# Kernel optimization log

Measured on AMD Instinct MI355X. Metric: run time of the kernel, lower is better.

## Reference

```python
import jax, jax.numpy as jnp
import numpy as np

PATCH = 16  # conv kernel size == stride


def _patch_embed(im, W, b):
    # im: (B, C, H, W) NCHW; W: (hidden, C, s, s); returns (B, h, w, hidden)
    out = jax.lax.conv_general_dilated(
        im, W, window_strides=(PATCH, PATCH), padding='VALID',
        dimension_numbers=('NCHW', 'OIHW', 'NCHW'))
    out = out + b[None, :, None, None]
    return jnp.transpose(out, (0, 2, 3, 1))  # (B, h, w, hidden)


def setup_inputs() -> dict:
    key = jax.random.key(0)
    k1, k2, k3, k4 = jax.random.split(key, 4)
    B, C, H, Wd = 64, 3, 224, 224
    hidden = 384
    x = jax.random.normal(k1, (B, C, H, Wd), dtype=jnp.float32)
    y = jax.random.normal(k2, (B, C, H, Wd), dtype=jnp.float32)
    fan_in = C * PATCH * PATCH
    bound = 1.0 / np.sqrt(fan_in)
    W = jax.random.uniform(k3, (hidden, C, PATCH, PATCH), dtype=jnp.float32,
                           minval=-bound, maxval=bound)
    b = jax.random.uniform(k4, (hidden,), dtype=jnp.float32,
                           minval=-bound, maxval=bound)
    return {'x': x, 'y': y, 'W': W, 'b': b}


def reference(x, y, W, b):
    B = x.shape[0]
    xp = _patch_embed(x, W, b)  # (B, h, w, C)
    yp = _patch_embed(y, W, b)  # (B, h, w, C)
    h, w = xp.shape[1], xp.shape[2]
    logp = jax.nn.log_softmax(xp, axis=-1)          # (B, h, w, C)
    q = jax.lax.stop_gradient(jax.nn.softmax(yp, axis=-1))  # detached targets
    # CE[i, j] = mean over (h, w) of -(q_j * logp_i).sum(-1)
    # Faithful factorization of the (B, B, h, w, C) broadcast in the original.
    CE = -jnp.einsum('ihwc,jhwc->ij', logp, q) / (h * w)  # (B, B)
    close = jnp.trace(CE) / B
    far = (CE.sum() - jnp.trace(CE)) / (B * B - B)
    return close / far
```

## Files before the change

### kernel.cpp

```cpp
#include <hip/hip_runtime.h>

#define HID   384
#define K_PE  768
#define IMGST 150528
#define POS   196

typedef unsigned short ushort_t;
using f32x4  = __attribute__((ext_vector_type(4))) float;
using short8 = __attribute__((ext_vector_type(8))) short;

__device__ __forceinline__ unsigned bfpack(float lo, float hi) {
    union { float f; unsigned u; } a, b; a.f = lo; b.f = hi;
    unsigned ra = (a.u + 0x7fffu + ((a.u >> 16) & 1u)) >> 16;
    unsigned rb = (b.u + 0x7fffu + ((b.u >> 16) & 1u)) & 0xffff0000u;
    return ra | rb;
}

__global__ __launch_bounds__(256) void prep(const float* __restrict__ W,
                                            ushort_t* __restrict__ Wfrag,
                                            float* __restrict__ scal) {
    const int t = blockIdx.x * 256 + threadIdx.x;
    if (t < 4) scal[t] = 0.f;
    const int n  = t / 96;
    const int ko = t - n * 96;
    const float4 a  = *(const float4*)(W + (size_t)n * K_PE + ko * 8);
    const float4 bb = *(const float4*)(W + (size_t)n * K_PE + ko * 8 + 4);
    uint4 pq;
    pq.x = bfpack(a.x, a.y);   pq.y = bfpack(a.z, a.w);
    pq.z = bfpack(bb.x, bb.y); pq.w = bfpack(bb.z, bb.w);
    const int nt    = n >> 4;
    const int kc    = ko >> 2;
    const int lanew = (ko & 3) * 16 + (n & 15);
    ((uint4*)Wfrag)[(nt * 24 + kc) * 64 + lanew] = pq;
}

__global__ __launch_bounds__(256, 2) void pef(
    const float* __restrict__ x, const float* __restrict__ y,
    const ushort_t* __restrict__ Wfrag, const float* __restrict__ bias,
    float* __restrict__ scal, float* __restrict__ Lg, float* __restrict__ Qg) {
    const int blk = blockIdx.x;
    const int pi  = blk >> 5;
    const int ig  = blk & 31;

    __shared__ __align__(16) ushort_t As[2][1792];
    __shared__ float Smx[4][32], Ssx[4][32], Smy[4][32], Ssy[4][32];
    __shared__ float sT[4];

    const int tid  = threadIdx.x;
    const int wave = tid >> 6;
    const int lane = tid & 63;
    const int lm   = lane & 15;
    const int lq   = lane >> 4;

    const int rr   = tid >> 5;
    const int sj   = tid & 31;
    const int st   = rr >> 2;
    const int simg = (rr >> 1) & 1;
    const int skh  = rr & 1;
    const int sq   = sj & 1;
    const int spj  = sj >> 1;
    const bool sact = sj < 28;
    const float* srow = (st ? y : x) +
        (size_t)(ig * 2 + simg) * IMGST + pi * 3584 + sj * 8;
    const int aoff = (((skh * 2 + sq) * 2 + st) * 2 + simg) * 112 + spj * 8;

    int ard[2][2];
#pragma unroll
    for (int t = 0; t < 2; ++t)
#pragma unroll
        for (int mi = 0; mi < 2; ++mi) {
            int m = mi * 16 + lm; if (m > 27) m = 27;
            const int img = (m >= 14) ? 1 : 0;
            const int pj  = m - img * 14;
            ard[t][mi] = ((lq * 2 + t) * 2 + img) * 112 + pj * 8;
        }

    f32x4 accx[2][6] = {};
    f32x4 accy[2][6] = {};

    if (sact) {
        const float4 f0 = *(const float4*)(srow + skh * 224);
        const float4 f1 = *(const float4*)(srow + skh * 224 + 4);
        uint4 px;
        px.x = bfpack(f0.x, f0.y); px.y = bfpack(f0.z, f0.w);
        px.z = bfpack(f1.x, f1.y); px.w = bfpack(f1.z, f1.w);
        *(uint4*)&As[0][aoff] = px;
    }
    short8 bfr[6];
#pragma unroll
    for (int ni = 0; ni < 6; ++ni)
        bfr[ni] = *(const short8*)(Wfrag +
                  (size_t)(((wave * 6 + ni) * 24) * 64 + lane) * 8);
    __syncthreads();

#pragma unroll 2
    for (int kk = 0; kk < 24; ++kk) {
        const int cur = kk & 1;
        const int kn  = (kk < 23) ? kk + 1 : 0;
        const int off = (kn >> 3) * 50176 + ((kn & 7) * 2 + skh) * 224;
        float4 f0{}, f1{};
        if (sact) {
            f0 = *(const float4*)(srow + off);
            f1 = *(const float4*)(srow + off + 4);
        }
        short8 bfrn[6];
#pragma unroll
        for (int ni = 0; ni < 6; ++ni)
            bfrn[ni] = *(const short8*)(Wfrag +
                       (size_t)(((wave * 6 + ni) * 24 + kn) * 64 + lane) * 8);
        short8 af[2][2];
#pragma unroll
        for (int t = 0; t < 2; ++t)
#pragma unroll
            for (int mi = 0; mi < 2; ++mi)
                af[t][mi] = *(const short8*)&As[cur][ard[t][mi]];
#pragma unroll
        for (int mi = 0; mi < 2; ++mi)
#pragma unroll
            for (int ni = 0; ni < 6; ++ni) {
                accx[mi][ni] = __builtin_amdgcn_mfma_f32_16x16x32_bf16(
                    af[0][mi], bfr[ni], accx[mi][ni], 0, 0, 0);
                accy[mi][ni] = __builtin_amdgcn_mfma_f32_16x16x32_bf16(
                    af[1][mi], bfr[ni], accy[mi][ni], 0, 0, 0);
            }
        if (sact) {
            uint4 px;
            px.x = bfpack(f0.x, f0.y); px.y = bfpack(f0.z, f0.w);
            px.z = bfpack(f1.x, f1.y); px.w = bfpack(f1.z, f1.w);
            *(uint4*)&As[cur ^ 1][aoff] = px;
        }
#pragma unroll
        for (int ni = 0; ni < 6; ++ni) bfr[ni] = bfrn[ni];
        __syncthreads();
    }

#pragma unroll
    for (int ni = 0; ni < 6; ++ni) {
        const float bv = bias[wave * 96 + ni * 16 + lm];
#pragma unroll
        for (int mi = 0; mi < 2; ++mi)
#pragma unroll
            for (int r = 0; r < 4; ++r) {
                accx[mi][ni][r] += bv;
                accy[mi][ni][r] += bv;
            }
    }

    float mx[2][4], my_[2][4];
#pragma unroll
    for (int mi = 0; mi < 2; ++mi)
#pragma unroll
        for (int r = 0; r < 4; ++r) {
            float a = accx[mi][0][r], bb = accy[mi][0][r];
#pragma unroll
            for (int ni = 1; ni < 6; ++ni) {
                a  = fmaxf(a,  accx[mi][ni][r]);
                bb = fmaxf(bb, accy[mi][ni][r]);
            }
            mx[mi][r] = a; my_[mi][r] = bb;
        }
#pragma unroll
    for (int off = 1; off < 16; off <<= 1)
#pragma unroll
        for (int mi = 0; mi < 2; ++mi)
#pragma unroll
            for (int r = 0; r < 4; ++r) {
                mx[mi][r]  = fmaxf(mx[mi][r],  __shfl_xor(mx[mi][r],  off));
                my_[mi][r] = fmaxf(my_[mi][r], __shfl_xor(my_[mi][r], off));
            }
    if (lm == 0)
#pragma unroll
        for (int mi = 0; mi < 2; ++mi)
#pragma unroll
            for (int r = 0; r < 4; ++r) {
                Smx[wave][mi * 16 + lq * 4 + r] = mx[mi][r];
                Smy[wave][mi * 16 + lq * 4 + r] = my_[mi][r];
            }
    __syncthreads();
#pragma unroll
    for (int mi = 0; mi < 2; ++mi)
#pragma unroll
        for (int r = 0; r < 4; ++r) {
            const int row = mi * 16 + lq * 4 + r;
            mx[mi][r]  = fmaxf(fmaxf(Smx[0][row], Smx[1][row]),
                               fmaxf(Smx[2][row], Smx[3][row]));
            my_[mi][r] = fmaxf(fmaxf(Smy[0][row], Smy[1][row]),
                               fmaxf(Smy[2][row], Smy[3][row]));
        }

    float sx[2][4], sy[2][4];
#pragma unroll
    for (int mi = 0; mi < 2; ++mi)
#pragma unroll
        for (int r = 0; r < 4; ++r) {
            float a = 0.f, bb = 0.f;
#pragma unroll
            for (int ni = 0; ni < 6; ++ni) {
                a  += __expf(accx[mi][ni][r] - mx[mi][r]);
                bb += __expf(accy[mi][ni][r] - my_[mi][r]);
            }
            sx[mi][r] = a; sy[mi][r] = bb;
        }
#pragma unroll
    for (int off = 1; off < 16; off <<= 1)
#pragma unroll
        for (int mi = 0; mi < 2; ++mi)
#pragma unroll
            for (int r = 0; r < 4; ++r) {
                sx[mi][r] += __shfl_xor(sx[mi][r], off);
                sy[mi][r] += __shfl_xor(sy[mi][r], off);
            }
    if (lm == 0)
#pragma unroll
        for (int mi = 0; mi < 2; ++mi)
#pragma unroll
            for (int r = 0; r < 4; ++r) {
                Ssx[wave][mi * 16 + lq * 4 + r] = sx[mi][r];
                Ssy[wave][mi * 16 + lq * 4 + r] = sy[mi][r];
            }
    __syncthreads();
    float shx[2][4], invy[2][4];
#pragma unroll
    for (int mi = 0; mi < 2; ++mi)
#pragma unroll
        for (int r = 0; r < 4; ++r) {
            const int row = mi * 16 + lq * 4 + r;
            const float ssx = Ssx[0][row] + Ssx[1][row] + Ssx[2][row] + Ssx[3][row];
            const float ssy = Ssy[0][row] + Ssy[1][row] + Ssy[2][row] + Ssy[3][row];
            shx[mi][r]  = mx[mi][r] + __logf(ssx);
            invy[mi][r] = 1.f / ssy;
        }

    float T = 0.f;
#pragma unroll
    for (int mi = 0; mi < 2; ++mi)
#pragma unroll
        for (int r = 0; r < 4; ++r) {
            const int m = mi * 16 + lq * 4 + r;
            if (m < 28) {
                const int img = (m >= 14) ? 1 : 0;
                const int pj  = m - img * 14;
                const size_t lb = ((size_t)(pi * 64 + ig * 2 + img) * 14 + pj) * 384
                                  + wave * 96 + lm;
                const float sh  = shx[mi][r];
                const float mm  = my_[mi][r];
                const float inv = invy[mi][r];
#pragma unroll
                for (int ni = 0; ni < 6; ++ni) {
                    const float lp = accx[mi][ni][r] - sh;
                    const float qv = __expf(accy[mi][ni][r] - mm) * inv;
                    T += lp * qv;
                    Lg[lb + ni * 16] = lp;
                    Qg[lb + ni * 16] = qv;
                }
            }
        }
#pragma unroll
    for (int off = 32; off > 0; off >>= 1) T += __shfl_xor(T, off);
    if (lane == 0) sT[wave] = T;
    __syncthreads();
    if (tid == 0) atomicAdd(&scal[0], sT[0] + sT[1] + sT[2] + sT[3]);
}

__global__ __launch_bounds__(384) void fin(const float* __restrict__ Lg,
                                           const float* __restrict__ Qg,
                                           float* __restrict__ scal,
                                           float* __restrict__ out) {
    const int p  = blockIdx.x;
    const int pi = p / 14;
    const int pj = p - pi * 14;
    const int c  = threadIdx.x;
    float L = 0.f, Q = 0.f;
#pragma unroll 4
    for (int img = 0; img < 64; ++img) {
        const size_t o = ((size_t)(pi * 64 + img) * 14 + pj) * 384 + c;
        L += Lg[o];
        Q += Qg[o];
    }
    float s = L * Q;
#pragma unroll
    for (int off = 32; off > 0; off >>= 1) s += __shfl_xor(s, off);
    __shared__ float sw[6];
    if ((c & 63) == 0) sw[c >> 6] = s;
    __syncthreads();
    if (c == 0) {
        const float Sp = sw[0] + sw[1] + sw[2] + sw[3] + sw[4] + sw[5];
        atomicAdd(&scal[1], Sp);
        __threadfence();
        const int old = atomicAdd((int*)&scal[3], 1);
        if (old == POS - 1) {
            const float T = atomicAdd(&scal[0], 0.f);
            const float S = atomicAdd(&scal[1], 0.f);
            out[0] = 63.f * T / (S - T);
        }
    }
}

extern "C" void kernel_launch(void* const* d_in, const int* in_sizes, int n_in,
                              void* d_out, int out_size, void* d_ws, size_t ws_size,
                              hipStream_t stream) {
    const float* x = (const float*)d_in[0];
    const float* y = (const float*)d_in[1];
    const float* W = (const float*)d_in[2];
    const float* b = (const float*)d_in[3];
    float* out = (float*)d_out;

    char* ws = (char*)d_ws;
    float*    scal  = (float*)ws;
    ushort_t* Wfrag = (ushort_t*)(ws + 1024);
    float*    Lg    = (float*)(ws + 590848);
    float*    Qg    = (float*)(ws + 19858432);

    prep<<<144, 256, 0, stream>>>(W, Wfrag, scal);
    pef<<<448, 256, 0, stream>>>(x, y, Wfrag, b, scal, Lg, Qg);
    fin<<<196, 384, 0, stream>>>(Lg, Qg, scal, out);
}
```

Measured before the change: 151.0 us.

## Load A fragments directly from global into registers, drop LDS staging

The patch-embed GEMM kernel stops staging input pixels through double-buffered shared memory with per-iteration barriers. Each lane now loads its own MFMA A-fragment straight from global memory and converts it with the hardware packed bf16 conversion instruction, using a register double-buffer across unrolled k-steps. The finalize kernel doubles its threads so each position's 64-image reduction is split across two halves. The cost is that each wave loads the shared A data redundantly and register pressure rises, which may reduce occupancy.

Result: slower. 159.2 us (+5.5%).

```diff
diff --git a/kernel.cpp b/kernel.cpp
--- a/kernel.cpp
+++ b/kernel.cpp
@@ -15,6 +15,12 @@
     unsigned rb = (b.u + 0x7fffu + ((b.u >> 16) & 1u)) & 0xffff0000u;
     return ra | rb;
 }
+__device__ __forceinline__ unsigned cvtpk(float lo, float hi) {
+    unsigned r;
+    asm("v_cvt_pk_bf16_f32 %0, %1, %2" : "=v"(r) : "v"(lo), "v"(hi));
+    return r;
+}
+union S8u { unsigned u[4]; short8 s; };
 
 __global__ __launch_bounds__(256) void prep(const float* __restrict__ W,
                                             ushort_t* __restrict__ Wfrag,
@@ -42,7 +48,6 @@
     const int pi  = blk >> 5;
     const int ig  = blk & 31;
 
-    __shared__ __align__(16) ushort_t As[2][1792];
     __shared__ float Smx[4][32], Ssx[4][32], Smy[4][32], Ssy[4][32];
     __shared__ float sT[4];
 
@@ -52,87 +57,73 @@
     const int lm   = lane & 15;
     const int lq   = lane >> 4;
 
-    const int rr   = tid >> 5;
-    const int sj   = tid & 31;
-    const int st   = rr >> 2;
-    const int simg = (rr >> 1) & 1;
-    const int skh  = rr & 1;
-    const int sq   = sj & 1;
-    const int spj  = sj >> 1;
-    const bool sact = sj < 28;
-    const float* srow = (st ? y : x) +
-        (size_t)(ig * 2 + simg) * IMGST + pi * 3584 + sj * 8;
-    const int aoff = (((skh * 2 + sq) * 2 + st) * 2 + simg) * 112 + spj * 8;
-
-    int ard[2][2];
-#pragma unroll
-    for (int t = 0; t < 2; ++t)
-#pragma unroll
-        for (int mi = 0; mi < 2; ++mi) {
-            int m = mi * 16 + lm; if (m > 27) m = 27;
-            const int img = (m >= 14) ? 1 : 0;
-            const int pj  = m - img * 14;
-            ard[t][mi] = ((lq * 2 + t) * 2 + img) * 112 + pj * 8;
-        }
+    const float* sp[4];
+#pragma unroll
+    for (int f = 0; f < 4; ++f) {
+        const int t = f >> 1, mi = f & 1;
+        int m = mi * 16 + lm; if (m > 27) m = 27;
+        const int img = (m >= 14) ? 1 : 0;
+        const int pj  = m - img * 14;
+        sp[f] = (t ? y : x) + (size_t)(ig * 2 + img) * IMGST
+              + (pi * 16 + (lq >> 1)) * 224 + pj * 16 + (lq & 1) * 8;
+    }
 
     f32x4 accx[2][6] = {};
     f32x4 accy[2][6] = {};
 
-    if (sact) {
-        const float4 f0 = *(const float4*)(srow + skh * 224);
-        const float4 f1 = *(const float4*)(srow + skh * 224 + 4);
-        uint4 px;
-        px.x = bfpack(f0.x, f0.y); px.y = bfpack(f0.z, f0.w);
-        px.z = bfpack(f1.x, f1.y); px.w = bfpack(f1.z, f1.w);
-        *(uint4*)&As[0][aoff] = px;
-    }
-    short8 bfr[6];
-#pragma unroll
-    for (int ni = 0; ni < 6; ++ni)
-        bfr[ni] = *(const short8*)(Wfrag +
-                  (size_t)(((wave * 6 + ni) * 24) * 64 + lane) * 8);
-    __syncthreads();
-
-#pragma unroll 2
-    for (int kk = 0; kk < 24; ++kk) {
-        const int cur = kk & 1;
-        const int kn  = (kk < 23) ? kk + 1 : 0;
-        const int off = (kn >> 3) * 50176 + ((kn & 7) * 2 + skh) * 224;
-        float4 f0{}, f1{};
-        if (sact) {
-            f0 = *(const float4*)(srow + off);
-            f1 = *(const float4*)(srow + off + 4);
-        }
-        short8 bfrn[6];
-#pragma unroll
-        for (int ni = 0; ni < 6; ++ni)
-            bfrn[ni] = *(const short8*)(Wfrag +
-                       (size_t)(((wave * 6 + ni) * 24 + kn) * 64 + lane) * 8);
-        short8 af[2][2];
-#pragma unroll
-        for (int t = 0; t < 2; ++t)
-#pragma unroll
-            for (int mi = 0; mi < 2; ++mi)
-                af[t][mi] = *(const short8*)&As[cur][ard[t][mi]];
-#pragma unroll
-        for (int mi = 0; mi < 2; ++mi)
-#pragma unroll
-            for (int ni = 0; ni < 6; ++ni) {
-                accx[mi][ni] = __builtin_amdgcn_mfma_f32_16x16x32_bf16(
-                    af[0][mi], bfr[ni], accx[mi][ni], 0, 0, 0);
-                accy[mi][ni] = __builtin_amdgcn_mfma_f32_16x16x32_bf16(
-                    af[1][mi], bfr[ni], accy[mi][ni], 0, 0, 0);
-            }
-        if (sact) {
-            uint4 px;
-            px.x = bfpack(f0.x, f0.y); px.y = bfpack(f0.z, f0.w);
-            px.z = bfpack(f1.x, f1.y); px.w = bfpack(f1.z, f1.w);
-            *(uint4*)&As[cur ^ 1][aoff] = px;
-        }
-#pragma unroll
-        for (int ni = 0; ni < 6; ++ni) bfr[ni] = bfrn[ni];
-        __syncthreads();
-    }
+#define LOADA(F, KN)                                                          \
+    {                                                                         \
+        const int off_ = ((KN) >> 3) * 50176 + ((KN) & 7) * 448;              \
+        _Pragma("unroll")                                                     \
+        for (int f = 0; f < 4; ++f) {                                         \
+            F[2 * f]     = *(const float4*)(sp[f] + off_);                    \
+            F[2 * f + 1] = *(const float4*)(sp[f] + off_ + 4);                \
+        }                                                                     \
+    }
+#define LOADB(B, KN)                                                          \
+    {                                                                         \
+        _Pragma("unroll")                                                     \
+        for (int ni = 0; ni < 6; ++ni)                                        \
+            B[ni] = *(const short8*)(Wfrag +                                  \
+                    ((size_t)((wave * 6 + ni) * 24 + (KN)) * 64 + lane) * 8); \
+    }
+#define STEP(F, B)                                                            \
+    {                                                                         \
+        short8 af[4];                                                         \
+        _Pragma("unroll")                                                     \
+        for (int f = 0; f < 4; ++f) {                                         \
+            S8u u_;                                                           \
+            u_.u[0] = cvtpk(F[2 * f].x, F[2 * f].y);                          \
+            u_.u[1] = cvtpk(F[2 * f].z, F[2 * f].w);                          \
+            u_.u[2] = cvtpk(F[2 * f + 1].x, F[2 * f + 1].y);                  \
+            u_.u[3] = cvtpk(F[2 * f + 1].z, F[2 * f + 1].w);                  \
+            af[f] = u_.s;                                                     \
+        }                                                                     \
+        _Pragma("unroll")                                                     \
+        for (int mi = 0; mi < 2; ++mi)                                        \
+            _Pragma("unroll")                                                 \
+            for (int ni = 0; ni < 6; ++ni) {                                  \
+                accx[mi][ni] = __builtin_amdgcn_mfma_f32_16x16x32_bf16(       \
+                    af[mi], B[ni], accx[mi][ni], 0, 0, 0);                    \
+                accy[mi][ni] = __builtin_amdgcn_mfma_f32_16x16x32_bf16(       \
+                    af[2 + mi], B[ni], accy[mi][ni], 0, 0, 0);                \
+            }                                                                 \
+    }
+
+    float4 fA[8], fB[8];
+    short8 bA[6], bB[6];
+    LOADA(fA, 0) LOADB(bA, 0)
+    for (int kk2 = 0; kk2 < 12; ++kk2) {
+        const int k1 = kk2 * 2 + 1;
+        const int k2 = (k1 < 23) ? k1 + 1 : 0;
+        LOADA(fB, k1) LOADB(bB, k1)
+        STEP(fA, bA)
+        LOADA(fA, k2) LOADB(bA, k2)
+        STEP(fB, bB)
+    }
+#undef LOADA
+#undef LOADB
+#undef STEP
 
 #pragma unroll
     for (int ni = 0; ni < 6; ++ni) {
@@ -262,29 +253,38 @@
     if (tid == 0) atomicAdd(&scal[0], sT[0] + sT[1] + sT[2] + sT[3]);
 }
 
-__global__ __launch_bounds__(384) void fin(const float* __restrict__ Lg,
+__global__ __launch_bounds__(768) void fin(const float* __restrict__ Lg,
                                            const float* __restrict__ Qg,
                                            float* __restrict__ scal,
                                            float* __restrict__ out) {
     const int p  = blockIdx.x;
     const int pi = p / 14;
     const int pj = p - pi * 14;
-    const int c  = threadIdx.x;
+    const int t  = threadIdx.x;
+    const int h  = t / 384;
+    const int c  = t - h * 384;
     float L = 0.f, Q = 0.f;
 #pragma unroll 4
-    for (int img = 0; img < 64; ++img) {
+    for (int i = 0; i < 32; ++i) {
+        const int img = h * 32 + i;
         const size_t o = ((size_t)(pi * 64 + img) * 14 + pj) * 384 + c;
         L += Lg[o];
         Q += Qg[o];
     }
-    float s = L * Q;
+    __shared__ float LL[384], QQ[384];
+    if (h == 0) { LL[c] = L; QQ[c] = Q; }
+    __syncthreads();
+    float s = 0.f;
+    if (h == 1) s = (LL[c] + L) * (QQ[c] + Q);
 #pragma unroll
     for (int off = 32; off > 0; off >>= 1) s += __shfl_xor(s, off);
-    __shared__ float sw[6];
-    if ((c & 63) == 0) sw[c >> 6] = s;
-    __syncthreads();
-    if (c == 0) {
-        const float Sp = sw[0] + sw[1] + sw[2] + sw[3] + sw[4] + sw[5];
+    __shared__ float sw[12];
+    if ((t & 63) == 0) sw[t >> 6] = s;
+    __syncthreads();
+    if (t == 0) {
+        float Sp = 0.f;
+#pragma unroll
+        for (int w = 0; w < 12; ++w) Sp += sw[w];
         atomicAdd(&scal[1], Sp);
         __threadfence();
         const int old = atomicAdd((int*)&scal[3], 1);
@@ -313,5 +313,5 @@
 
     prep<<<144, 256, 0, stream>>>(W, Wfrag, scal);
     pef<<<448, 256, 0, stream>>>(x, y, Wfrag, b, scal, Lg, Qg);
-    fin<<<196, 384, 0, stream>>>(Lg, Qg, scal, out);
-}
+    fin<<<196, 768, 0, stream>>>(Lg, Qg, scal, out);
+}
```

## Pack logp/q as bf16 pairs, double K-step per iteration, contiguous fin layout

Applied to the files above, without the earlier changes.

The intermediate logp and q tensors are packed into a single 32-bit word of two bf16 values with v_cvt_pk_bf16_f32, halving the write and read traffic between pef and fin. The layout is reordered so each fin block reads a contiguous slab, and fin uses 768 threads split over two image halves. The pef main loop now stages two K-chunks per iteration with a larger LDS buffer, halving the number of barriers. Rounding the intermediates to bf16 adds precision loss to the final ratio.

Measured after the change: 136.6 us. 9.6% less time.

```diff
diff --git a/kernel.cpp b/kernel.cpp
--- a/kernel.cpp
+++ b/kernel.cpp
@@ -14,6 +14,14 @@
     unsigned ra = (a.u + 0x7fffu + ((a.u >> 16) & 1u)) >> 16;
     unsigned rb = (b.u + 0x7fffu + ((b.u >> 16) & 1u)) & 0xffff0000u;
     return ra | rb;
+}
+__device__ __forceinline__ unsigned cvtpk(float lo, float hi) {
+    unsigned r;
+    asm("v_cvt_pk_bf16_f32 %0, %1, %2" : "=v"(r) : "v"(lo), "v"(hi));
+    return r;
+}
+__device__ __forceinline__ float bf2f(unsigned hibits) {
+    union { unsigned u; float f; } v; v.u = hibits; return v.f;
 }
 
 __global__ __launch_bounds__(256) void prep(const float* __restrict__ W,
@@ -37,12 +45,12 @@
 __global__ __launch_bounds__(256, 2) void pef(
     const float* __restrict__ x, const float* __restrict__ y,
     const ushort_t* __restrict__ Wfrag, const float* __restrict__ bias,
-    float* __restrict__ scal, float* __restrict__ Lg, float* __restrict__ Qg) {
+    float* __restrict__ scal, unsigned* __restrict__ Zg) {
     const int blk = blockIdx.x;
     const int pi  = blk >> 5;
     const int ig  = blk & 31;
 
-    __shared__ __align__(16) ushort_t As[2][1792];
+    __shared__ __align__(16) ushort_t As[2][8 * 456];
     __shared__ float Smx[4][32], Ssx[4][32], Smy[4][32], Ssy[4][32];
     __shared__ float sT[4];
 
@@ -61,8 +69,10 @@
     const int spj  = sj >> 1;
     const bool sact = sj < 28;
     const float* srow = (st ? y : x) +
-        (size_t)(ig * 2 + simg) * IMGST + pi * 3584 + sj * 8;
-    const int aoff = (((skh * 2 + sq) * 2 + st) * 2 + simg) * 112 + spj * 8;
+        (size_t)(ig * 2 + simg) * IMGST + pi * 3584 + skh * 224 + sj * 8;
+    const int ainner = st * 224 + simg * 112 + spj * 8;
+    const int aoff0  = (skh * 2 + sq) * 456 + ainner;
+    const int aoff1  = ((skh + 2) * 2 + sq) * 456 + ainner;
 
     int ard[2][2];
 #pragma unroll
@@ -72,67 +82,93 @@
             int m = mi * 16 + lm; if (m > 27) m = 27;
             const int img = (m >= 14) ? 1 : 0;
             const int pj  = m - img * 14;
-            ard[t][mi] = ((lq * 2 + t) * 2 + img) * 112 + pj * 8;
-        }
+            ard[t][mi] = t * 224 + img * 112 + pj * 8;
+        }
+    const int ob0 = lq * 456, ob1 = (4 + lq) * 456;
 
     f32x4 accx[2][6] = {};
     f32x4 accy[2][6] = {};
 
+#define LOADB(B, KC)                                                          \
+    {                                                                         \
+        _Pragma("unroll")                                                     \
+        for (int ni = 0; ni < 6; ++ni)                                        \
+            B[ni] = *(const short8*)(Wfrag +                                  \
+                    ((size_t)((wave * 6 + ni) * 24 + (KC)) * 64 + lane) * 8); \
+    }
+#define MFMA24(AF, B, ACX, ACY)                                               \
+    {                                                                         \
+        _Pragma("unroll")                                                     \
+        for (int mi = 0; mi < 2; ++mi)                                        \
+            _Pragma("unroll")                                                 \
+            for (int ni = 0; ni < 6; ++ni) {                                  \
+                ACX[mi][ni] = __builtin_amdgcn_mfma_f32_16x16x32_bf16(        \
+                    AF[0][mi], B[ni], ACX[mi][ni], 0, 0, 0);                  \
+                ACY[mi][ni] = __builtin_amdgcn_mfma_f32_16x16x32_bf16(        \
+                    AF[1][mi], B[ni], ACY[mi][ni], 0, 0, 0);                  \
+            }                                                                 \
+    }
+
     if (sact) {
-        const float4 f0 = *(const float4*)(srow + skh * 224);
-        const float4 f1 = *(const float4*)(srow + skh * 224 + 4);
-        uint4 px;
-        px.x = bfpack(f0.x, f0.y); px.y = bfpack(f0.z, f0.w);
-        px.z = bfpack(f1.x, f1.y); px.w = bfpack(f1.z, f1.w);
-        *(uint4*)&As[0][aoff] = px;
-    }
-    short8 bfr[6];
-#pragma unroll
-    for (int ni = 0; ni < 6; ++ni)
-        bfr[ni] = *(const short8*)(Wfrag +
-                  (size_t)(((wave * 6 + ni) * 24) * 64 + lane) * 8);
+        const float4 f0 = *(const float4*)(srow);
+        const float4 f1 = *(const float4*)(srow + 4);
+        const float4 f2 = *(const float4*)(srow + 448);
+        const float4 f3 = *(const float4*)(srow + 452);
+        uint4 p0, p1;
+        p0.x = bfpack(f0.x, f0.y); p0.y = bfpack(f0.z, f0.w);
+        p0.z = bfpack(f1.x, f1.y); p0.w = bfpack(f1.z, f1.w);
+        p1.x = bfpack(f2.x, f2.y); p1.y = bfpack(f2.z, f2.w);
+        p1.z = bfpack(f3.x, f3.y); p1.w = bfpack(f3.z, f3.w);
+        *(uint4*)&As[0][aoff0] = p0;
+        *(uint4*)&As[0][aoff1] = p1;
+    }
+    short8 b0[6], b1[6], bn[6];
+    LOADB(b0, 0)
     __syncthreads();
 
 #pragma unroll 2
-    for (int kk = 0; kk < 24; ++kk) {
+    for (int kk = 0; kk < 12; ++kk) {
         const int cur = kk & 1;
-        const int kn  = (kk < 23) ? kk + 1 : 0;
-        const int off = (kn >> 3) * 50176 + ((kn & 7) * 2 + skh) * 224;
-        float4 f0{}, f1{};
-        if (sact) {
-            f0 = *(const float4*)(srow + off);
-            f1 = *(const float4*)(srow + off + 4);
-        }
-        short8 bfrn[6];
-#pragma unroll
-        for (int ni = 0; ni < 6; ++ni)
-            bfrn[ni] = *(const short8*)(Wfrag +
-                       (size_t)(((wave * 6 + ni) * 24 + kn) * 64 + lane) * 8);
+        const bool have = sact && (kk < 11);
+        const int nb = ((kk + 1) >> 2) * 50176 + ((kk + 1) & 3) * 896;
+        float4 f0{}, f1{}, f2{}, f3{};
+        if (have) {
+            f0 = *(const float4*)(srow + nb);
+            f1 = *(const float4*)(srow + nb + 4);
+            f2 = *(const float4*)(srow + nb + 448);
+            f3 = *(const float4*)(srow + nb + 452);
+        }
+        LOADB(b1, kk * 2 + 1)
         short8 af[2][2];
 #pragma unroll
         for (int t = 0; t < 2; ++t)
 #pragma unroll
             for (int mi = 0; mi < 2; ++mi)
-                af[t][mi] = *(const short8*)&As[cur][ard[t][mi]];
-#pragma unroll
-        for (int mi = 0; mi < 2; ++mi)
-#pragma unroll
-            for (int ni = 0; ni < 6; ++ni) {
-                accx[mi][ni] = __builtin_amdgcn_mfma_f32_16x16x32_bf16(
-                    af[0][mi], bfr[ni], accx[mi][ni], 0, 0, 0);
-                accy[mi][ni] = __builtin_amdgcn_mfma_f32_16x16x32_bf16(
-                    af[1][mi], bfr[ni], accy[mi][ni], 0, 0, 0);
-            }
-        if (sact) {
-            uint4 px;
-            px.x = bfpack(f0.x, f0.y); px.y = bfpack(f0.z, f0.w);
-            px.z = bfpack(f1.x, f1.y); px.w = bfpack(f1.z, f1.w);
-            *(uint4*)&As[cur ^ 1][aoff] = px;
-        }
-#pragma unroll
-        for (int ni = 0; ni < 6; ++ni) bfr[ni] = bfrn[ni];
+                af[t][mi] = *(const short8*)&As[cur][ob0 + ard[t][mi]];
+        MFMA24(af, b0, accx, accy)
+        const int kn2 = (kk < 11) ? (kk + 1) * 2 : 0;
+        LOADB(bn, kn2)
+#pragma unroll
+        for (int t = 0; t < 2; ++t)
+#pragma unroll
+            for (int mi = 0; mi < 2; ++mi)
+                af[t][mi] = *(const short8*)&As[cur][ob1 + ard[t][mi]];
+        MFMA24(af, b1, accx, accy)
+        if (have) {
+            uint4 p0, p1;
+            p0.x = bfpack(f0.x, f0.y); p0.y = bfpack(f0.z, f0.w);
+            p0.z = bfpack(f1.x, f1.y); p0.w = bfpack(f1.z, f1.w);
+            p1.x = bfpack(f2.x, f2.y); p1.y = bfpack(f2.z, f2.w);
+            p1.z = bfpack(f3.x, f3.y); p1.w = bfpack(f3.z, f3.w);
+            *(uint4*)&As[cur ^ 1][aoff0] = p0;
+            *(uint4*)&As[cur ^ 1][aoff1] = p1;
+        }
+#pragma unroll
+        for (int ni = 0; ni < 6; ++ni) b0[ni] = bn[ni];
         __syncthreads();
     }
+#undef LOADB
+#undef MFMA24
 
 #pragma unroll
     for (int ni = 0; ni < 6; ++ni) {
@@ -240,7 +276,7 @@
             if (m < 28) {
                 const int img = (m >= 14) ? 1 : 0;
                 const int pj  = m - img * 14;
-                const size_t lb = ((size_t)(pi * 64 + ig * 2 + img) * 14 + pj) * 384
+                const size_t lb = ((size_t)(pi * 14 + pj) * 64 + ig * 2 + img) * 384
                                   + wave * 96 + lm;
                 const float sh  = shx[mi][r];
                 const float mm  = my_[mi][r];
@@ -250,8 +286,7 @@
                     const float lp = accx[mi][ni][r] - sh;
                     const float qv = __expf(accy[mi][ni][r] - mm) * inv;
                     T += lp * qv;
-                    Lg[lb + ni * 16] = lp;
-                    Qg[lb + ni * 16] = qv;
+                    Zg[lb + ni * 16] = cvtpk(lp, qv);
                 }
             }
         }
@@ -262,29 +297,34 @@
     if (tid == 0) atomicAdd(&scal[0], sT[0] + sT[1] + sT[2] + sT[3]);
 }
 
-__global__ __launch_bounds__(384) void fin(const float* __restrict__ Lg,
-                                           const float* __restrict__ Qg,
+__global__ __launch_bounds__(768) void fin(const unsigned* __restrict__ Zg,
                                            float* __restrict__ scal,
                                            float* __restrict__ out) {
-    const int p  = blockIdx.x;
-    const int pi = p / 14;
-    const int pj = p - pi * 14;
-    const int c  = threadIdx.x;
+    const int p = blockIdx.x;
+    const int t = threadIdx.x;
+    const int h = t / 384;
+    const int c = t - h * 384;
     float L = 0.f, Q = 0.f;
 #pragma unroll 4
-    for (int img = 0; img < 64; ++img) {
-        const size_t o = ((size_t)(pi * 64 + img) * 14 + pj) * 384 + c;
-        L += Lg[o];
-        Q += Qg[o];
-    }
-    float s = L * Q;
+    for (int i = 0; i < 32; ++i) {
+        const unsigned u = Zg[((size_t)p * 64 + h * 32 + i) * 384 + c];
+        L += bf2f(u << 16);
+        Q += bf2f(u & 0xffff0000u);
+    }
+    __shared__ float LL[384], QQ[384];
+    if (h == 0) { LL[c] = L; QQ[c] = Q; }
+    __syncthreads();
+    float s = 0.f;
+    if (h == 1) s = (LL[c] + L) * (QQ[c] + Q);
 #pragma unroll
     for (int off = 32; off > 0; off >>= 1) s += __shfl_xor(s, off);
-    __shared__ float sw[6];
-    if ((c & 63) == 0) sw[c >> 6] = s;
-    __syncthreads();
-    if (c == 0) {
-        const float Sp = sw[0] + sw[1] + sw[2] + sw[3] + sw[4] + sw[5];
+    __shared__ float sw[12];
+    if ((t & 63) == 0) sw[t >> 6] = s;
+    __syncthreads();
+    if (t == 0) {
+        float Sp = 0.f;
+#pragma unroll
+        for (int w = 0; w < 12; ++w) Sp += sw[w];
         atomicAdd(&scal[1], Sp);
         __threadfence();
         const int old = atomicAdd((int*)&scal[3], 1);
@@ -308,10 +348,9 @@
     char* ws = (char*)d_ws;
     float*    scal  = (float*)ws;
     ushort_t* Wfrag = (ushort_t*)(ws + 1024);
-    float*    Lg    = (float*)(ws + 590848);
-    float*    Qg    = (float*)(ws + 19858432);
+    unsigned* Zg    = (unsigned*)(ws + 590848);
 
     prep<<<144, 256, 0, stream>>>(W, Wfrag, scal);
-    pef<<<448, 256, 0, stream>>>(x, y, Wfrag, b, scal, Lg, Qg);
-    fin<<<196, 384, 0, stream>>>(Lg, Qg, scal, out);
-}
+    pef<<<448, 256, 0, stream>>>(x, y, Wfrag, b, scal, Zg);
+    fin<<<196, 768, 0, stream>>>(Zg, scal, out);
+}
```
